# Optimization experiments

Hardware: AMD Instinct MI355X
Metric: run time of the kernel (lower is better)

## Reference

```python
import jax, jax.numpy as jnp
import numpy as np

H = 4        # num_heads
HD = 64      # head_dim
BD = 40      # bias_dim
QDIM = 256
KDIM = 256
VDIM = 256
NQ = 1024
NK = 1024
NEG = -9e15


def mish(x):
    return x * jnp.tanh(jax.nn.softplus(x))


def layer_norm(x, g, b, eps=1e-5):
    m = jnp.mean(x, axis=-1, keepdims=True)
    v = jnp.var(x, axis=-1, keepdims=True)
    return (x - m) / jnp.sqrt(v + eps) * g + b


def _xavier(key, fi, fo):
    lim = np.sqrt(6.0 / (fi + fo)).astype(np.float32)
    return jax.random.uniform(key, (fi, fo), minval=-lim, maxval=lim, dtype=jnp.float32)


def setup_inputs() -> dict:
    key = jax.random.key(0)
    ks = jax.random.split(key, 12)
    D = H * HD
    inp = {
        'q': jax.random.normal(ks[0], (NQ, QDIM), jnp.float32),
        'k': jax.random.normal(ks[1], (NK, KDIM), jnp.float32),
        'v': jax.random.normal(ks[2], (NK, VDIM), jnp.float32),
        'bias': jax.random.normal(ks[3], (NQ, NK, BD), jnp.float32),
        'mask': jax.random.randint(ks[4], (NQ, NK), 0, 2, jnp.int32),
        # projections (weights stored [in, out]; biases zero-init as in torch code)
        'Wq': _xavier(ks[5], QDIM, D), 'bq': jnp.zeros((D,), jnp.float32),
        'Wk': _xavier(ks[6], KDIM, D), 'bk': jnp.zeros((D,), jnp.float32),
        'Wbias': _xavier(ks[7], BD, H * BD), 'bbias': jnp.zeros((H * BD,), jnp.float32),
        'Wqo': _xavier(ks[8], D, QDIM), 'bqo': jnp.zeros((QDIM,), jnp.float32),
        'Wko': _xavier(ks[9], D, KDIM), 'bko': jnp.zeros((KDIM,), jnp.float32),
        'g_q': jnp.ones((QDIM,), jnp.float32), 'be_q': jnp.zeros((QDIM,), jnp.float32),
        'g_k': jnp.ones((KDIM,), jnp.float32), 'be_k': jnp.zeros((KDIM,), jnp.float32),
        'Wbo': _xavier(ks[10], BD * H, BD), 'bbo': jnp.zeros((BD,), jnp.float32),
    }
    return inp


def reference(q, k, v, bias, mask, Wq, bq, Wk, bk, Wbias, bbias, Wqo, bqo,
              Wko, bko, g_q, be_q, g_k, be_k, Wbo, bbo):
    nq, nk = q.shape[0], k.shape[0]
    # per-head projections: [H, N, HD]
    proj_q = (q @ Wq + bq).reshape(nq, H, HD).transpose(1, 0, 2)
    proj_k = (k @ Wk + bk).reshape(nk, H, HD).transpose(1, 0, 2)
    # values are raw v broadcast over heads (v_proj is unused in original forward)
    proj_v = jnp.broadcast_to(v[None], (H, nk, v.shape[-1]))

    # distance-bias: project then per-head L2 norm -> [H, Nq, Nk]
    biasp = bias @ Wbias + bbias                          # [Nq, Nk, H*BD]
    diffs = jnp.linalg.norm(biasp.reshape(nq, nk, H, BD), axis=-1).transpose(2, 0, 1)

    logits = jnp.einsum('hqd,hkd->hqk', proj_q, proj_k) / np.float32(np.sqrt(HD))
    logits = logits + diffs
    logits = jnp.where(mask[None] == 0, jnp.float32(NEG), logits)
    attn = jax.nn.softmax(logits, axis=-1)
    values = jnp.einsum('hqk,hkv->hqv', attn, proj_v)      # [H, Nq, VDIM]
    values = values.transpose(1, 0, 2).reshape(nq, H * v.shape[-1])

    # note the (N, HD, H) flatten order, matching torch permute(1,2,0).reshape
    pq = proj_q.transpose(1, 2, 0).reshape(nq, HD * H)
    pk = proj_k.transpose(1, 2, 0).reshape(nk, HD * H)
    q_out = layer_norm(q + mish(pq @ Wqo + bqo), g_q, be_q)
    k_out = layer_norm(k + mish(pk @ Wko + bko), g_k, be_k)

    vals_mean = jnp.mean(values, axis=-1, keepdims=True)   # [Nq, 1]
    bias_out = mish(biasp @ Wbo + bbo)                     # [Nq, Nk, BD]
    return (q_out, k_out, vals_mean, bias_out)
```

## Files before the change

kernel.cpp:

```cpp
#include <hip/hip_runtime.h>
#include <hip/hip_bf16.h>
#include <math.h>

#define NEGV -9e15f

typedef short bf16x8 __attribute__((ext_vector_type(8)));
typedef float f32x4 __attribute__((ext_vector_type(4)));

__device__ __forceinline__ unsigned short f2bf(float x) {
  unsigned u = __float_as_uint(x);
  u += 0x7fffu + ((u >> 16) & 1u);
  return (unsigned short)(u >> 16);
}

__device__ __forceinline__ unsigned pk2(float a, float b) {
  __hip_bfloat162 h = __float22bfloat162_rn(make_float2(a, b));
  unsigned u;
  __builtin_memcpy(&u, &h, 4);
  return u;
}

__device__ __forceinline__ float mishf(float x) {
  float u = __expf(fminf(x, 30.0f));
  float n = u * (u + 2.0f);
  return x * __fdividef(n, n + 2.0f);
}

#define KEEP4(v) asm volatile("" : "+v"((v).x), "+v"((v).y), "+v"((v).z), "+v"((v).w))

__global__ void prep_kernel(const float* __restrict__ v, float* __restrict__ s,
                            const float* __restrict__ Wb, const float* __restrict__ bb,
                            const float* __restrict__ Wo, float* __restrict__ M) {
  int bid = blockIdx.x;
  int lane = threadIdx.x;
  if (bid < 1024) {
    float4 a = *reinterpret_cast<const float4*>(v + (size_t)bid * 256 + lane * 4);
    float x = a.x + a.y + a.z + a.w;
    for (int off = 32; off; off >>= 1) x += __shfl_down(x, off);
    if (lane == 0) s[bid] = x;
  } else {
    int i = bid - 1024;
    if (lane >= 40) return;
    float acc = 0.0f;
    for (int k = 0; k < 160; ++k) {
      float w = (i < 40) ? Wb[i * 160 + k] : bb[k];
      acc = fmaf(w, Wo[k * 40 + lane], acc);
    }
    M[i * 40 + lane] = acc;
  }
}

__global__ __launch_bounds__(256) void gemm_pair(
    const float* __restrict__ A0, const float* __restrict__ W0,
    const float* __restrict__ bv0, float* __restrict__ C0,
    const float* __restrict__ A1, const float* __restrict__ W1,
    const float* __restrict__ bv1, float* __restrict__ C1, int perm) {
  const float* A = blockIdx.z ? A1 : A0;
  const float* W = blockIdx.z ? W1 : W0;
  const float* bvec = blockIdx.z ? bv1 : bv0;
  float* C = blockIdx.z ? C1 : C0;
  __shared__ float sAT[16][68];
  __shared__ float sW[16][68];
  int tid = threadIdx.x;
  int c0 = blockIdx.x * 64, r0 = blockIdx.y * 64;
  int ty = tid >> 4, tx = tid & 15;
  float acc[4][4] = {};
  for (int k0 = 0; k0 < 256; k0 += 16) {
    {
      int r = tid >> 2, jq = tid & 3;
      float4 a4 = *reinterpret_cast<const float4*>(A + (size_t)(r0 + r) * 256 + k0 + jq * 4);
      sAT[jq * 4 + 0][r] = a4.x;
      sAT[jq * 4 + 1][r] = a4.y;
      sAT[jq * 4 + 2][r] = a4.z;
      sAT[jq * 4 + 3][r] = a4.w;
    }
    {
      int kk = tid >> 4, cq = tid & 15;
      int gk = k0 + kk;
      int row = perm ? ((gk & 63) * 4 + (gk >> 6)) : gk;
      float4 w4 = *reinterpret_cast<const float4*>(W + (size_t)row * 256 + c0 + cq * 4);
      *reinterpret_cast<float4*>(&sW[kk][cq * 4]) = w4;
    }
    __syncthreads();
#pragma unroll
    for (int kk = 0; kk < 16; ++kk) {
      float4 av = *reinterpret_cast<const float4*>(&sAT[kk][ty * 4]);
      float4 bv = *reinterpret_cast<const float4*>(&sW[kk][tx * 4]);
      float a[4] = {av.x, av.y, av.z, av.w};
      float b[4] = {bv.x, bv.y, bv.z, bv.w};
#pragma unroll
      for (int i = 0; i < 4; ++i)
#pragma unroll
        for (int j = 0; j < 4; ++j) acc[i][j] = fmaf(a[i], b[j], acc[i][j]);
    }
    __syncthreads();
  }
#pragma unroll
  for (int i = 0; i < 4; ++i) {
    int rr = r0 + ty * 4 + i, cc = c0 + tx * 4;
    float4 o;
    o.x = acc[i][0] + bvec[cc + 0];
    o.y = acc[i][1] + bvec[cc + 1];
    o.z = acc[i][2] + bvec[cc + 2];
    o.w = acc[i][3] + bvec[cc + 3];
    *reinterpret_cast<float4*>(C + (size_t)rr * 256 + cc) = o;
  }
}

__global__ __launch_bounds__(256) void ln_pair(
    const float* __restrict__ x0q, const float* __restrict__ yq,
    const float* __restrict__ gq, const float* __restrict__ beq,
    float* __restrict__ outq,
    const float* __restrict__ x0k, const float* __restrict__ yk,
    const float* __restrict__ gk, const float* __restrict__ bek,
    float* __restrict__ outk) {
  const float* x0 = blockIdx.y ? x0k : x0q;
  const float* y  = blockIdx.y ? yk  : yq;
  const float* g  = blockIdx.y ? gk  : gq;
  const float* be = blockIdx.y ? bek : beq;
  float* out      = blockIdx.y ? outk : outq;
  __shared__ float r1[5], r2[5];
  int r = blockIdx.x, t = threadIdx.x;
  int wid = t >> 6, lane = t & 63;
  float x = x0[(size_t)r * 256 + t] + mishf(y[(size_t)r * 256 + t]);
  float a = x, b = x * x;
  for (int off = 32; off; off >>= 1) {
    a += __shfl_down(a, off);
    b += __shfl_down(b, off);
  }
  if (lane == 0) { r1[wid] = a; r2[wid] = b; }
  __syncthreads();
  if (t == 0) {
    r1[4] = r1[0] + r1[1] + r1[2] + r1[3];
    r2[4] = r2[0] + r2[1] + r2[2] + r2[3];
  }
  __syncthreads();
  float m = r1[4] * (1.0f / 256.0f);
  float var = r2[4] * (1.0f / 256.0f) - m * m;
  out[(size_t)r * 256 + t] = (x - m) * rsqrtf(var + 1e-5f) * g[t] + be[t];
}

__global__ __launch_bounds__(256, 4) void bias_mfma(
    const float* __restrict__ bias, const float* __restrict__ Wb,
    const float* __restrict__ bb, const float* __restrict__ Mmat,
    const float* __restrict__ bo, float* __restrict__ diffs,
    float* __restrict__ bout) {
  __shared__ unsigned short wfL[20 * 64 * 8];
  __shared__ unsigned short mfL[6 * 64 * 8];
  int tid = threadIdx.x;
  int wv = tid >> 6, lane = tid & 63;
  int r = lane & 15, g = lane >> 4;

  for (int idx = tid; idx < 20 * 64; idx += 256) {
    int grp = idx >> 6, lid = idx & 63;
    int n0 = grp >> 1, ks = grp & 1;
    int rr = lid & 15, gg = lid >> 4;
    int c = n0 * 16 + rr;
    unsigned short tmp[8];
#pragma unroll
    for (int jj = 0; jj < 8; ++jj) {
      int k = ks * 32 + gg * 8 + jj;
      float w = (k < 40) ? Wb[k * 160 + c] : ((k == 40) ? bb[c] : 0.0f);
      tmp[jj] = f2bf(w);
    }
    *reinterpret_cast<uint4*>(&wfL[idx * 8]) = *reinterpret_cast<const uint4*>(tmp);
  }
  for (int idx = tid; idx < 6 * 64; idx += 256) {
    int grp = idx >> 6, lid = idx & 63;
    int n = grp >> 1, ks = grp & 1;
    int rr = lid & 15, gg = lid >> 4;
    int c = n * 16 + rr;
    unsigned short tmp[8];
#pragma unroll
    for (int jj = 0; jj < 8; ++jj) {
      int k = ks * 32 + gg * 8 + jj;
      float w = (k <= 40 && c < 40) ? Mmat[k * 40 + c] : 0.0f;
      tmp[jj] = f2bf(w);
    }
    *reinterpret_cast<uint4*>(&mfL[idx * 8]) = *reinterpret_cast<const uint4*>(tmp);
  }
  f32x4 bo40, bo41, bo42;
  {
    float4 t0 = *reinterpret_cast<const float4*>(bo + 4 * g);
    float4 t1 = *reinterpret_cast<const float4*>(bo + 16 + 4 * g);
    bo40[0] = t0.x; bo40[1] = t0.y; bo40[2] = t0.z; bo40[3] = t0.w;
    bo41[0] = t1.x; bo41[1] = t1.y; bo41[2] = t1.z; bo41[3] = t1.w;
    if (g < 2) {
      float4 t2 = *reinterpret_cast<const float4*>(bo + 32 + 4 * g);
      bo42[0] = t2.x; bo42[1] = t2.y; bo42[2] = t2.z; bo42[3] = t2.w;
    } else {
      bo42[0] = 0.0f; bo42[1] = 0.0f; bo42[2] = 0.0f; bo42[3] = 0.0f;
    }
  }
  __syncthreads();

  size_t row0 = ((size_t)blockIdx.x * 4 + wv) * 256;

  const float* xr = bias + (row0 + r) * 40;
  float4 xA = *reinterpret_cast<const float4*>(xr + g * 8);
  float4 xB = *reinterpret_cast<const float4*>(xr + g * 8 + 4);
  float4 xC = *reinterpret_cast<const float4*>(xr + 32);
  float4 xD = *reinterpret_cast<const float4*>(xr + 36);
  KEEP4(xA); KEEP4(xB); KEEP4(xC); KEEP4(xD);

#pragma unroll 1
  for (int t = 0; t < 16; ++t) {
    const size_t p0 = row0 + (size_t)t * 16;
    bf16x8 xf0, xf1;
    {
      uint4 t0 = {pk2(xA.x, xA.y), pk2(xA.z, xA.w), pk2(xB.x, xB.y), pk2(xB.z, xB.w)};
      unsigned d0 = (g == 1) ? 0x00003f80u : pk2(xC.x, xC.y);
      uint4 t1 = {d0, pk2(xC.z, xC.w), pk2(xD.x, xD.y), pk2(xD.z, xD.w)};
      __builtin_memcpy(&xf0, &t0, 16);
      __builtin_memcpy(&xf1, &t1, 16);
    }
    if (t < 15) {
      const float* xr2 = bias + (p0 + 16 + r) * 40;
      xA = *reinterpret_cast<const float4*>(xr2 + g * 8);
      xB = *reinterpret_cast<const float4*>(xr2 + g * 8 + 4);
      xC = *reinterpret_cast<const float4*>(xr2 + 32);
      xD = *reinterpret_cast<const float4*>(xr2 + 36);
      KEEP4(xA); KEEP4(xB); KEEP4(xC); KEEP4(xD);
    }
    float cs[10];
#pragma unroll
    for (int n0 = 0; n0 < 10; ++n0) {
      bf16x8 wa = *reinterpret_cast<const bf16x8*>(&wfL[((n0 * 2 + 0) * 64 + lane) * 8]);
      bf16x8 wb2 = *reinterpret_cast<const bf16x8*>(&wfL[((n0 * 2 + 1) * 64 + lane) * 8]);
      f32x4 q = {0.0f, 0.0f, 0.0f, 0.0f};
      q = __builtin_amdgcn_mfma_f32_16x16x32_bf16(wa, xf0, q, 0, 0, 0);
      q = __builtin_amdgcn_mfma_f32_16x16x32_bf16(wb2, xf1, q, 0, 0, 0);
      cs[n0] = q[0] * q[0] + q[1] * q[1] + q[2] * q[2] + q[3] * q[3];
    }
    float hv0 = cs[0] + cs[1] + ((g < 2) ? cs[2] : 0.0f);
    float hv1 = ((g < 2) ? 0.0f : cs[2]) + cs[3] + cs[4];
    float hv2 = cs[5] + cs[6] + ((g < 2) ? cs[7] : 0.0f);
    float hv3 = ((g < 2) ? 0.0f : cs[7]) + cs[8] + cs[9];
    hv0 += __shfl_xor(hv0, 16); hv0 += __shfl_xor(hv0, 32);
    hv1 += __shfl_xor(hv1, 16); hv1 += __shfl_xor(hv1, 32);
    hv2 += __shfl_xor(hv2, 16); hv2 += __shfl_xor(hv2, 32);
    hv3 += __shfl_xor(hv3, 16); hv3 += __shfl_xor(hv3, 32);
    float ss = (g == 0) ? hv0 : (g == 1) ? hv1 : (g == 2) ? hv2 : hv3;
    diffs[(size_t)g * (1024 * 1024) + p0 + r] = sqrtf(ss);
    f32x4 o0 = bo40, o1 = bo41, o2 = bo42;
    {
      bf16x8 m00 = *reinterpret_cast<const bf16x8*>(&mfL[((0 * 2 + 0) * 64 + lane) * 8]);
      bf16x8 m01 = *reinterpret_cast<const bf16x8*>(&mfL[((0 * 2 + 1) * 64 + lane) * 8]);
      bf16x8 m10 = *reinterpret_cast<const bf16x8*>(&mfL[((1 * 2 + 0) * 64 + lane) * 8]);
      bf16x8 m11 = *reinterpret_cast<const bf16x8*>(&mfL[((1 * 2 + 1) * 64 + lane) * 8]);
      bf16x8 m20 = *reinterpret_cast<const bf16x8*>(&mfL[((2 * 2 + 0) * 64 + lane) * 8]);
      bf16x8 m21 = *reinterpret_cast<const bf16x8*>(&mfL[((2 * 2 + 1) * 64 + lane) * 8]);
      o0 = __builtin_amdgcn_mfma_f32_16x16x32_bf16(m00, xf0, o0, 0, 0, 0);
      o1 = __builtin_amdgcn_mfma_f32_16x16x32_bf16(m10, xf0, o1, 0, 0, 0);
      o2 = __builtin_amdgcn_mfma_f32_16x16x32_bf16(m20, xf0, o2, 0, 0, 0);
      o0 = __builtin_amdgcn_mfma_f32_16x16x32_bf16(m01, xf1, o0, 0, 0, 0);
      o1 = __builtin_amdgcn_mfma_f32_16x16x32_bf16(m11, xf1, o1, 0, 0, 0);
      o2 = __builtin_amdgcn_mfma_f32_16x16x32_bf16(m21, xf1, o2, 0, 0, 0);
    }
    float* bp = bout + (size_t)(p0 + r) * 40;
    float4 st;
    st.x = mishf(o0[0]); st.y = mishf(o0[1]);
    st.z = mishf(o0[2]); st.w = mishf(o0[3]);
    *reinterpret_cast<float4*>(bp + 4 * g) = st;
    st.x = mishf(o1[0]); st.y = mishf(o1[1]);
    st.z = mishf(o1[2]); st.w = mishf(o1[3]);
    *reinterpret_cast<float4*>(bp + 16 + 4 * g) = st;
    if (g < 2) {
      st.x = mishf(o2[0]); st.y = mishf(o2[1]);
      st.z = mishf(o2[2]); st.w = mishf(o2[3]);
      *reinterpret_cast<float4*>(bp + 32 + 4 * g) = st;
    }
  }
}

__global__ __launch_bounds__(256) void qk_softmax(
    const float* __restrict__ pq, const float* __restrict__ pk,
    const int* __restrict__ mask, const float* __restrict__ diffs,
    const float* __restrict__ sv, float* __restrict__ mpart,
    float* __restrict__ spart, float* __restrict__ dpart) {
  __shared__ float sQT[64][68];
  __shared__ float sKT[64][68];
  int tid = threadIdx.x;
  int k0 = blockIdx.x * 64, q0 = blockIdx.y * 64, h = blockIdx.z;
  for (int i = tid; i < 1024; i += 256) {
    int r = i >> 4, dq = i & 15;
    float4 a = *reinterpret_cast<const float4*>(pq + (size_t)(q0 + r) * 256 + h * 64 + dq * 4);
    sQT[dq * 4 + 0][r] = a.x;
    sQT[dq * 4 + 1][r] = a.y;
    sQT[dq * 4 + 2][r] = a.z;
    sQT[dq * 4 + 3][r] = a.w;
    float4 b = *reinterpret_cast<const float4*>(pk + (size_t)(k0 + r) * 256 + h * 64 + dq * 4);
    sKT[dq * 4 + 0][r] = b.x;
    sKT[dq * 4 + 1][r] = b.y;
    sKT[dq * 4 + 2][r] = b.z;
    sKT[dq * 4 + 3][r] = b.w;
  }
  __syncthreads();
  int ty = tid >> 4, tx = tid & 15;
  float acc[4][4] = {};
#pragma unroll 4
  for (int d = 0; d < 64; ++d) {
    float4 av = *reinterpret_cast<const float4*>(&sQT[d][ty * 4]);
    float4 bv = *reinterpret_cast<const float4*>(&sKT[d][tx * 4]);
    float a[4] = {av.x, av.y, av.z, av.w};
    float b[4] = {bv.x, bv.y, bv.z, bv.w};
#pragma unroll
    for (int i = 0; i < 4; ++i)
#pragma unroll
      for (int j = 0; j < 4; ++j) acc[i][j] = fmaf(a[i], b[j], acc[i][j]);
  }
  float4 s4 = *reinterpret_cast<const float4*>(sv + k0 + tx * 4);
#pragma unroll
  for (int i = 0; i < 4; ++i) {
    int qq = q0 + ty * 4 + i;
    size_t base = (size_t)h * 1048576 + (size_t)qq * 1024 + k0 + tx * 4;
    float4 dv = *reinterpret_cast<const float4*>(diffs + base);
    int4 mv = *reinterpret_cast<const int4*>(mask + (size_t)qq * 1024 + k0 + tx * 4);
    float l0 = mv.x ? fmaf(acc[i][0], 0.125f, dv.x) : NEGV;
    float l1 = mv.y ? fmaf(acc[i][1], 0.125f, dv.y) : NEGV;
    float l2 = mv.z ? fmaf(acc[i][2], 0.125f, dv.z) : NEGV;
    float l3 = mv.w ? fmaf(acc[i][3], 0.125f, dv.w) : NEGV;
    float tm = fmaxf(fmaxf(l0, l1), fmaxf(l2, l3));
    tm = fmaxf(tm, __shfl_xor(tm, 1));
    tm = fmaxf(tm, __shfl_xor(tm, 2));
    tm = fmaxf(tm, __shfl_xor(tm, 4));
    tm = fmaxf(tm, __shfl_xor(tm, 8));
    float e0 = mv.x ? __expf(l0 - tm) : 0.0f;
    float e1 = mv.y ? __expf(l1 - tm) : 0.0f;
    float e2 = mv.z ? __expf(l2 - tm) : 0.0f;
    float e3 = mv.w ? __expf(l3 - tm) : 0.0f;
    float ps = e0 + e1 + e2 + e3;
    float pd = e0 * s4.x + e1 * s4.y + e2 * s4.z + e3 * s4.w;
    ps += __shfl_xor(ps, 1); pd += __shfl_xor(pd, 1);
    ps += __shfl_xor(ps, 2); pd += __shfl_xor(pd, 2);
    ps += __shfl_xor(ps, 4); pd += __shfl_xor(pd, 4);
    ps += __shfl_xor(ps, 8); pd += __shfl_xor(pd, 8);
    if (tx == 0) {
      int plane = (h * 16 + blockIdx.x) * 1024 + qq;
      mpart[plane] = tm;
      spart[plane] = ps;
      dpart[plane] = pd;
    }
  }
}

__global__ void vm_reduce(const float* __restrict__ mpart,
                          const float* __restrict__ spart,
                          const float* __restrict__ dpart,
                          float* __restrict__ vm) {
  int q = blockIdx.x * 256 + threadIdx.x;
  float accum = 0.0f;
#pragma unroll
  for (int h = 0; h < 4; ++h) {
    float M = -3e38f;
#pragma unroll
    for (int kb = 0; kb < 16; ++kb)
      M = fmaxf(M, mpart[(h * 16 + kb) * 1024 + q]);
    float s = 0.0f, d = 0.0f;
#pragma unroll
    for (int kb = 0; kb < 16; ++kb) {
      int p = (h * 16 + kb) * 1024 + q;
      float sc = __expf(mpart[p] - M);
      s = fmaf(spart[p], sc, s);
      d = fmaf(dpart[p], sc, d);
    }
    accum += d / s;
  }
  vm[q] = accum * (1.0f / 1024.0f);
}

extern "C" void kernel_launch(void* const* d_in, const int* in_sizes, int n_in,
                              void* d_out, int out_size, void* d_ws, size_t ws_size,
                              hipStream_t stream) {
  const float* q     = (const float*)d_in[0];
  const float* k     = (const float*)d_in[1];
  const float* v     = (const float*)d_in[2];
  const float* bias  = (const float*)d_in[3];
  const int*   mask  = (const int*)d_in[4];
  const float* Wq    = (const float*)d_in[5];
  const float* bq    = (const float*)d_in[6];
  const float* Wk    = (const float*)d_in[7];
  const float* bk    = (const float*)d_in[8];
  const float* Wbias = (const float*)d_in[9];
  const float* bbias = (const float*)d_in[10];
  const float* Wqo   = (const float*)d_in[11];
  const float* bqo   = (const float*)d_in[12];
  const float* Wko   = (const float*)d_in[13];
  const float* bko   = (const float*)d_in[14];
  const float* g_q   = (const float*)d_in[15];
  const float* be_q  = (const float*)d_in[16];
  const float* g_k   = (const float*)d_in[17];
  const float* be_k  = (const float*)d_in[18];
  const float* Wbo   = (const float*)d_in[19];
  const float* bbo   = (const float*)d_in[20];

  float* out = (float*)d_out;
  float* ws  = (float*)d_ws;
  float* projq = ws;
  float* projk = ws + 262144;
  float* qo    = ws + 524288;
  float* ko    = ws + 786432;
  float* diffs = ws + 1048576;
  float* svec  = ws + 5242880;
  float* Mmat  = ws + 5243904;
  float* mpart = ws + 5246976;
  float* spart = ws + 5312512;
  float* dpart = ws + 5378048;

  float* q_out    = out;
  float* k_out    = out + 262144;
  float* vmean    = out + 524288;
  float* bias_out = out + 525312;

  prep_kernel<<<1065, 64, 0, stream>>>(v, svec, Wbias, bbias, Wbo, Mmat);
  gemm_pair<<<dim3(4, 16, 2), 256, 0, stream>>>(q, Wq, bq, projq,
                                                k, Wk, bk, projk, 0);
  bias_mfma<<<1024, 256, 0, stream>>>(bias, Wbias, bbias, Mmat, bbo, diffs, bias_out);
  gemm_pair<<<dim3(4, 16, 2), 256, 0, stream>>>(projq, Wqo, bqo, qo,
                                                projk, Wko, bko, ko, 1);
  ln_pair<<<dim3(1024, 2), 256, 0, stream>>>(q, qo, g_q, be_q, q_out,
                                             k, ko, g_k, be_k, k_out);
  qk_softmax<<<dim3(16, 16, 4), 256, 0, stream>>>(projq, projk, mask, diffs,
                                                  svec, mpart, spart, dpart);
  vm_reduce<<<4, 256, 0, stream>>>(mpart, spart, dpart, vmean);
}
```

Before: 159.9 us.

## Replace FP32 tiled projection GEMMs with bf16 MFMA kernel

The small 1024x256x256 projection GEMM pair, which used scalar FP32 FMAs with shared-memory tiling, is replaced by a kernel using 16x16x32 bf16 MFMA instructions. Each block stages its full 256x64 weight slice into LDS as bf16, laid out in MFMA fragment order. Each wave loads its 16 input rows into registers and converts them to bf16, and the bias is folded into the accumulator init. This cuts ALU time in the two GEMM launches but lowers input precision to bf16, and the weight staging uses strided scalar global loads.

```diff
diff --git a/kernel.cpp b/kernel.cpp
--- a/kernel.cpp
+++ b/kernel.cpp
@@ -50,7 +50,7 @@
   }
 }
 
-__global__ __launch_bounds__(256) void gemm_pair(
+__global__ __launch_bounds__(256, 2) void gemm_mfma_pair(
     const float* __restrict__ A0, const float* __restrict__ W0,
     const float* __restrict__ bv0, float* __restrict__ C0,
     const float* __restrict__ A1, const float* __restrict__ W1,
@@ -59,51 +59,57 @@
   const float* W = blockIdx.z ? W1 : W0;
   const float* bvec = blockIdx.z ? bv1 : bv0;
   float* C = blockIdx.z ? C1 : C0;
-  __shared__ float sAT[16][68];
-  __shared__ float sW[16][68];
+  __shared__ unsigned short wT[4 * 8 * 64 * 8];
   int tid = threadIdx.x;
+  int wv = tid >> 6, lane = tid & 63;
+  int r = lane & 15, g = lane >> 4;
   int c0 = blockIdx.x * 64, r0 = blockIdx.y * 64;
-  int ty = tid >> 4, tx = tid & 15;
-  float acc[4][4] = {};
-  for (int k0 = 0; k0 < 256; k0 += 16) {
-    {
-      int r = tid >> 2, jq = tid & 3;
-      float4 a4 = *reinterpret_cast<const float4*>(A + (size_t)(r0 + r) * 256 + k0 + jq * 4);
-      sAT[jq * 4 + 0][r] = a4.x;
-      sAT[jq * 4 + 1][r] = a4.y;
-      sAT[jq * 4 + 2][r] = a4.z;
-      sAT[jq * 4 + 3][r] = a4.w;
-    }
-    {
-      int kk = tid >> 4, cq = tid & 15;
-      int gk = k0 + kk;
-      int row = perm ? ((gk & 63) * 4 + (gk >> 6)) : gk;
-      float4 w4 = *reinterpret_cast<const float4*>(W + (size_t)row * 256 + c0 + cq * 4);
-      *reinterpret_cast<float4*>(&sW[kk][cq * 4]) = w4;
-    }
-    __syncthreads();
-#pragma unroll
-    for (int kk = 0; kk < 16; ++kk) {
-      float4 av = *reinterpret_cast<const float4*>(&sAT[kk][ty * 4]);
-      float4 bv = *reinterpret_cast<const float4*>(&sW[kk][tx * 4]);
-      float a[4] = {av.x, av.y, av.z, av.w};
-      float b[4] = {bv.x, bv.y, bv.z, bv.w};
-#pragma unroll
-      for (int i = 0; i < 4; ++i)
-#pragma unroll
-        for (int j = 0; j < 4; ++j) acc[i][j] = fmaf(a[i], b[j], acc[i][j]);
-    }
-    __syncthreads();
-  }
-#pragma unroll
-  for (int i = 0; i < 4; ++i) {
-    int rr = r0 + ty * 4 + i, cc = c0 + tx * 4;
-    float4 o;
-    o.x = acc[i][0] + bvec[cc + 0];
-    o.y = acc[i][1] + bvec[cc + 1];
-    o.z = acc[i][2] + bvec[cc + 2];
-    o.w = acc[i][3] + bvec[cc + 3];
-    *reinterpret_cast<float4*>(C + (size_t)rr * 256 + cc) = o;
+
+  for (int idx = tid; idx < 4 * 8 * 64; idx += 256) {
+    int grp = idx >> 6, lid = idx & 63;
+    int n = grp >> 3, ks = grp & 7;
+    int cc = c0 + n * 16 + (lid & 15);
+    int kbase = ks * 32 + (lid >> 4) * 8;
+    unsigned short tmp[8];
+#pragma unroll
+    for (int jj = 0; jj < 8; ++jj) {
+      int k = kbase + jj;
+      int row = perm ? ((k & 63) * 4 + (k >> 6)) : k;
+      tmp[jj] = f2bf(W[row * 256 + cc]);
+    }
+    *reinterpret_cast<uint4*>(&wT[idx * 8]) = *reinterpret_cast<const uint4*>(tmp);
+  }
+  const float* xr = A + (size_t)(r0 + wv * 16 + r) * 256 + g * 8;
+  float4 xa[8], xb[8];
+#pragma unroll
+  for (int ks = 0; ks < 8; ++ks) {
+    xa[ks] = *reinterpret_cast<const float4*>(xr + ks * 32);
+    xb[ks] = *reinterpret_cast<const float4*>(xr + ks * 32 + 4);
+  }
+  f32x4 acc[4];
+#pragma unroll
+  for (int n = 0; n < 4; ++n) {
+    float4 b4 = *reinterpret_cast<const float4*>(bvec + c0 + n * 16 + 4 * g);
+    acc[n][0] = b4.x; acc[n][1] = b4.y; acc[n][2] = b4.z; acc[n][3] = b4.w;
+  }
+  __syncthreads();
+#pragma unroll
+  for (int ks = 0; ks < 8; ++ks) {
+    bf16x8 xf;
+    uint4 t = {pk2(xa[ks].x, xa[ks].y), pk2(xa[ks].z, xa[ks].w),
+               pk2(xb[ks].x, xb[ks].y), pk2(xb[ks].z, xb[ks].w)};
+    __builtin_memcpy(&xf, &t, 16);
+#pragma unroll
+    for (int n = 0; n < 4; ++n) {
+      bf16x8 wf = *reinterpret_cast<const bf16x8*>(&wT[((n * 8 + ks) * 64 + lane) * 8]);
+      acc[n] = __builtin_amdgcn_mfma_f32_16x16x32_bf16(wf, xf, acc[n], 0, 0, 0);
+    }
+  }
+  float* cp = C + (size_t)(r0 + wv * 16 + r) * 256 + c0;
+#pragma unroll
+  for (int n = 0; n < 4; ++n) {
+    float4 o = {acc[n][0], acc[n][1], acc[n][2], acc[n][3]};
+    *reinterpret_cast<float4*>(cp + n * 16 + 4 * g) = o;
   }
 }
 
@@ -413,11 +419,11 @@
   float* bias_out = out + 525312;
 
   prep_kernel<<<1065, 64, 0, stream>>>(v, svec, Wbias, bbias, Wbo, Mmat);
-  gemm_pair<<<dim3(4, 16, 2), 256, 0, stream>>>(q, Wq, bq, projq,
-                                                k, Wk, bk, projk, 0);
+  gemm_mfma_pair<<<dim3(4, 16, 2), 256, 0, stream>>>(q, Wq, bq, projq,
+                                                     k, Wk, bk, projk, 0);
   bias_mfma<<<1024, 256, 0, stream>>>(bias, Wbias, bbias, Mmat, bbo, diffs, bias_out);
-  gemm_pair<<<dim3(4, 16, 2), 256, 0, stream>>>(projq, Wqo, bqo, qo,
-                                                projk, Wko, bko, ko, 1);
+  gemm_mfma_pair<<<dim3(4, 16, 2), 256, 0, stream>>>(projq, Wqo, bqo, qo,
+                                                     projk, Wko, bko, ko, 1);
   ln_pair<<<dim3(1024, 2), 256, 0, stream>>>(q, qo, g_q, be_q, q_out,
                                              k, ko, g_k, be_k, k_out);
   qk_softmax<<<dim3(16, 16, 4), 256, 0, stream>>>(projq, projk, mask, diffs,
```

Result: faster. 141.0 us (-11.8%).
